# Optimization experiments

Measured on AMD Instinct MI355X. Metric: run time of the kernel, lower is better.

Reference implementation:

```python
import jax, jax.numpy as jnp
import numpy as np

BN_EPS = 1e-5

def _conv(x, w, bias=None):
    # x: [N,C,H,W], w: [O,I,3,3], SAME padding, stride 1
    y = jax.lax.conv_general_dilated(x, w, window_strides=(1, 1),
                                     padding=((1, 1), (1, 1)),
                                     dimension_numbers=('NCHW', 'OIHW', 'NCHW'))
    if bias is not None:
        y = y + bias[None, :, None, None]
    return y

def _cconv(xr, xi, wr, wi):
    # complex conv: (xr + i xi) * (wr + i wi), cross-term combination
    return _conv(xr, wr) - _conv(xi, wi), _conv(xr, wi) + _conv(xi, wr)

def _bn1(x, g, b):
    # per-channel batchnorm (training-style stats over N,H,W)
    mu = jnp.mean(x, axis=(0, 2, 3), keepdims=True)
    var = jnp.var(x, axis=(0, 2, 3), keepdims=True)
    xh = (x - mu) * jax.lax.rsqrt(var + BN_EPS)
    return xh * g[None, :, None, None] + b[None, :, None, None]

def _cbn(xr, xi, g, b):
    # naive complex BN: normalize real/imag parts separately, shared affine
    return _bn1(xr, g, b), _bn1(xi, g, b)

def _crelu(xr, xi):
    return jax.nn.relu(xr), jax.nn.relu(xi)

def setup_inputs() -> dict:
    key = jax.random.key(0)
    ks = jax.random.split(key, 16)
    def w(k, o, i, kh=3, kw=3, s=0.05):
        return jax.random.normal(k, (o, i, kh, kw), jnp.float32) * s
    d = {}
    d['x'] = jax.random.normal(ks[0], (4, 256, 128, 224), jnp.float32)
    d['w1r'] = w(ks[1], 144, 256); d['w1i'] = w(ks[2], 144, 256)
    d['g1'] = jnp.ones((144,), jnp.float32); d['b1'] = jnp.zeros((144,), jnp.float32)
    d['w2r'] = w(ks[3], 96, 144); d['w2i'] = w(ks[4], 96, 144)
    d['g2'] = jnp.ones((96,), jnp.float32); d['b2'] = jnp.zeros((96,), jnp.float32)
    d['w3r'] = w(ks[5], 96, 96); d['w3i'] = w(ks[6], 96, 96)
    d['g3'] = jnp.ones((96,), jnp.float32); d['b3'] = jnp.zeros((96,), jnp.float32)
    d['w4r'] = w(ks[7], 96, 96); d['w4i'] = w(ks[8], 96, 96)
    d['g4'] = jnp.ones((96,), jnp.float32); d['b4'] = jnp.zeros((96,), jnp.float32)
    d['wc'] = w(ks[9], 1, 96); d['bc'] = jnp.zeros((1,), jnp.float32)
    d['wg'] = w(ks[10], 2, 96); d['bg'] = jnp.zeros((2,), jnp.float32)
    return d

def reference(x, w1r, w1i, g1, b1, w2r, w2i, g2, b2,
              w3r, w3i, g3, b3, w4r, w4i, g4, b4, wc, bc, wg, bg):
    # real input promoted to complex with zero imag
    xr, xi = x, jnp.zeros_like(x)
    xr, xi = _cconv(xr, xi, w1r, w1i)
    xr, xi = _cbn(xr, xi, g1, b1)
    xr, xi = _crelu(xr, xi)
    xr, xi = _cconv(xr, xi, w2r, w2i)
    xr, xi = _cbn(xr, xi, g2, b2)
    xr, xi = _crelu(xr, xi)
    xr, xi = _cconv(xr, xi, w3r, w3i)
    xr, xi = _cbn(xr, xi, g3, b3)
    xr, xi = _crelu(xr, xi)
    xr, xi = _cconv(xr, xi, w4r, w4i)
    xr, xi = _cbn(xr, xi, g4, b4)
    xr, xi = _crelu(xr, xi)
    x_mag = jnp.sqrt(xr * xr + xi * xi)  # torch.abs on complex
    cls = jax.nn.sigmoid(_conv(x_mag, wc, bc))
    reg = _conv(x_mag, wg, bg)
    return jnp.concatenate([cls, reg], axis=1)  # [N, 1+reg_layer, H, W]
```

## Files before the change

### kernel.cpp

```cpp
#include <hip/hip_runtime.h>
#include <cstdint>
#include <cstddef>

#define P_TOT 114688
#define W_IMG 224
#define H_IMG 128
#define WP 228
#define HP 130

typedef _Float16 f16;
typedef __attribute__((ext_vector_type(8))) _Float16 f16x8;
typedef __attribute__((ext_vector_type(4))) _Float16 f16x4;
typedef __attribute__((ext_vector_type(4))) float f32x4;

#define WAITVM(N) asm volatile("s_waitcnt vmcnt(" #N ")" ::: "memory")

__device__ __forceinline__ void barrier_sync() {
  asm volatile("" ::: "memory");
  __builtin_amdgcn_s_barrier();
  asm volatile("" ::: "memory");
}

__device__ __forceinline__ void gload16(const void* g, void* l) {
  __builtin_amdgcn_global_load_lds((const __attribute__((address_space(1))) void*)g,
                                   (__attribute__((address_space(3))) void*)l, 16, 0, 0);
}

__device__ __forceinline__ size_t pad_px(int n, int h, int w) {
  return ((size_t)(n * HP + h + 1)) * WP + (w + 1);
}

__global__ void k_halo(f16* __restrict__ slab, int CS) {
  int c8n = CS >> 3;
  int tid = blockIdx.x * 256 + threadIdx.x;
  int c8 = tid % c8n;
  int rest = tid / c8n;
  if (rest >= 4 * 968) return;
  int n = rest / 968, i = rest % 968;
  int h, w;
  if (i < 456) { h = (i < 228) ? 0 : 129; w = i % 228; }
  else { int j = i - 456; h = 1 + (j >> 2); int k = j & 3; w = (k == 0) ? 0 : (224 + k); }
  size_t pp = ((size_t)(n * HP + h)) * WP + w;
  *(f16x8*)(slab + pp * CS + c8 * 8) = (f16x8){0, 0, 0, 0, 0, 0, 0, 0};
}

__global__ void k_pack_x(const float* __restrict__ x, f16* __restrict__ xb) {
  int tid = threadIdx.x;
  int pw  = tid & 15;
  int c8  = tid >> 4;
  int p   = blockIdx.x * 16 + pw;
  int w   = p % W_IMG;
  int h   = (p / W_IMG) % H_IMG;
  int n   = p / (H_IMG * W_IMG);
  const float* src = x + ((size_t)(n * 256 + c8 * 8) * H_IMG + h) * W_IMG + w;
  f16x8 v;
#pragma unroll
  for (int j = 0; j < 8; j++) v[j] = (f16)src[(size_t)j * (H_IMG * W_IMG)];
  int c8s = (c8 & ~3) | ((c8 ^ (w >> 1)) & 3);
  *(f16x8*)(xb + pad_px(n, h, w) * 256 + c8s * 8) = v;
}

__global__ void k_pack_w(const float* __restrict__ wa, const float* __restrict__ wb,
                         f16* __restrict__ dst, int mode, int OT, int CS,
                         int Coh, int Cih, int total) {
  int gid = blockIdx.x * 256 + threadIdx.x;
  if (gid >= total) return;
  int j  = gid & 31;
  int t1 = gid >> 5;
  int o  = t1 % OT;
  int t2 = t1 / OT;
  int CCc = CS >> 5;
  int cc = t2 % CCc;
  int kk = t2 / CCc;
  int chunkT = ((j >> 3) ^ (o >> 1)) & 3;
  int is = cc * 32 + chunkT * 8 + (j & 7);
  float val = 0.f;
  if (mode == 0) {
    val = (o < Coh) ? wa[((size_t)o * Cih + is) * 9 + kk]
                    : wb[((size_t)(o - Coh) * Cih + is) * 9 + kk];
  } else if (mode == 1) {
    if (o < Coh) {
      val = (is < Cih) ? wa[((size_t)o * Cih + is) * 9 + kk]
                       : -wb[((size_t)o * Cih + (is - Cih)) * 9 + kk];
    } else {
      int oo = o - Coh;
      val = (is < Cih) ? wb[((size_t)oo * Cih + is) * 9 + kk]
                       : wa[((size_t)oo * Cih + (is - Cih)) * 9 + kk];
    }
  } else {
    if (o == 0)      val = wa[(size_t)is * 9 + kk];
    else if (o == 1) val = wb[(size_t)is * 9 + kk];
    else if (o == 2) val = wb[(size_t)(96 + is) * 9 + kk];
  }
  dst[gid] = (f16)val;
}

template<int BM, int OT, int CS, int WM, int WN, bool HEAD>
__launch_bounds__(WM * WN * 64)
__global__ void k_gemm(const f16* __restrict__ xb, const f16* __restrict__ Apack,
                       f16* __restrict__ y, float* __restrict__ outh,
                       const float* __restrict__ bcp, const float* __restrict__ bgp,
                       float* __restrict__ sums, float* __restrict__ sumsq) {
  constexpr int NT = WM * WN * 64;
  constexpr int NWV = NT / 64;
  constexpr int CC = CS / 32;
  constexpr int MF = BM / (WM * 16);
  constexpr int NF = 224 / (WN * 16);
  constexpr int NCH = 9 * CC;
  constexpr int TILE1 = (BM + 224) * 32;
  constexpr int ACH = BM / 16;
  constexpr int TCH = ACH + 14;
  constexpr int NHALF = HEAD ? 1 : 2;
  static_assert(HEAD || (TCH % NWV == 0 && TCH / NWV == 5), "vmcnt math: 5 loads/thread/half");
  __shared__ f16 lds[2][NHALF * TILE1];

  constexpr int NOT = OT / BM;
  constexpr int nwg = NOT * 512;
  int bid = blockIdx.x;
  int swz = (bid & 7) * (nwg >> 3) + (bid >> 3);
  const int ot = swz % NOT;
  const int rq = swz / NOT;
  const int n = rq >> 7;
  const int h = rq & 127;
  const int tid  = threadIdx.x;
  const int lane = tid & 63;
  const int wv   = tid >> 6;
  const int wm   = wv % WM;
  const int wn   = wv / WM;
  const int obase  = wm * (MF * 16);
  const int wnbase = wn * (NF * 16);
  const int l15 = lane & 15;
  const int lhi = lane >> 4;
  const int aoff = l15 * 64 + (((lhi ^ (l15 >> 1)) & 3) << 4);

  f32x4 acc[MF][NF];
#pragma unroll
  for (int mi = 0; mi < MF; mi++)
#pragma unroll
    for (int ni = 0; ni < NF; ni++) acc[mi][ni] = (f32x4){0.f, 0.f, 0.f, 0.f};

  const char* abase = (const char*)Apack + (size_t)ot * BM * 64 + lane * 16;
  const char* bbase = (const char*)xb +
      (pad_px(n, h, 0) + (lane >> 2)) * (CS * 2) + (lane & 3) * 16;

  auto stage1 = [&](char* base, int q) {
    const int kk = q / CC, c = q % CC;
    const int dh = kk / 3 - 1;
    const int dw = kk % 3 - 1;
    const char* asrc = abase + (size_t)q * (OT * 64);
    const char* bsrc = bbase + (dh * WP + dw) * (int)(CS * 2) + c * 64;
#pragma unroll
    for (int ck = wv; ck < TCH; ck += NWV) {
      char* dst = base + ck * 1024;
      if (ck < ACH) gload16(asrc + ck * 1024, dst);
      else          gload16(bsrc + (size_t)(ck - ACH) * (16 * CS * 2), dst);
    }
  };

  auto compute_half = [&](const char* base, int kk) {
    const int dw = kk % 3 - 1;
    const char* Ab = base;
    const char* Bb = base + BM * 64;
    f16x8 af[MF], bfr[NF];
#pragma unroll
    for (int mi = 0; mi < MF; mi++)
      af[mi] = *(const f16x8*)(Ab + (obase + mi * 16) * 64 + aoff);
#pragma unroll
    for (int ni = 0; ni < NF; ni++) {
      int px = wnbase + ni * 16 + l15;
      int sw = ((lhi ^ ((px + dw) >> 1)) & 3) << 4;
      bfr[ni] = *(const f16x8*)(Bb + px * 64 + sw);
    }
    __builtin_amdgcn_s_setprio(1);
#pragma unroll
    for (int mi = 0; mi < MF; mi++)
#pragma unroll
      for (int ni = 0; ni < NF; ni++)
        acc[mi][ni] = __builtin_amdgcn_mfma_f32_16x16x32_f16(af[mi], bfr[ni], acc[mi][ni], 0, 0, 0);
    __builtin_amdgcn_s_setprio(0);
  };

  if constexpr (!HEAD) {
    constexpr int STEPS = (NCH + 1) / 2;
    auto stage_pair = [&](int buf, int q) {
      char* b = (char*)&lds[buf][0];
      int q1 = (q + 1 < NCH) ? (q + 1) : (NCH - 1);
      stage1(b, q);
      stage1(b + TILE1 * 2, q1);
    };
    stage_pair(0, 0);
    for (int s = 0; s < STEPS; ++s) {
      int qn = (s + 1) * 2;
      if (qn < NCH) { stage_pair((s + 1) & 1, qn); WAITVM(10); }
      else          { WAITVM(0); }
      barrier_sync();
      const char* b = (const char*)&lds[s & 1][0];
      int q = s * 2;
      compute_half(b, q / CC);
      if (q + 1 < NCH) compute_half(b + TILE1 * 2, (q + 1) / CC);
      barrier_sync();
    }
  } else {
    stage1((char*)&lds[0][0], 0);
    __syncthreads();
    int buf = 0;
    for (int t = 0; t < NCH; ++t) {
      int tn = t + 1;
      if (tn < NCH) stage1((char*)&lds[buf ^ 1][0], tn);
      compute_half((const char*)&lds[buf][0], t / CC);
      __syncthreads();
      buf ^= 1;
    }
  }

  if constexpr (!HEAD) {
    const size_t prow = pad_px(n, h, 0);
#pragma unroll
    for (int mi = 0; mi < MF; mi++) {
#pragma unroll
      for (int ni = 0; ni < NF; ni++) {
        int o = obase + mi * 16 + lhi * 4;
        int w = wnbase + ni * 16 + l15;
        f16x4 v4;
#pragma unroll
        for (int j = 0; j < 4; j++) v4[j] = (f16)acc[mi][ni][j];
        *(f16x4*)(y + (prow + w) * OT + ot * BM + o) = v4;
      }
    }
    float sv[MF][4], qv[MF][4];
#pragma unroll
    for (int mi = 0; mi < MF; mi++)
#pragma unroll
      for (int j = 0; j < 4; j++) {
        float s = 0.f, q = 0.f;
#pragma unroll
        for (int ni = 0; ni < NF; ni++) {
          float v = acc[mi][ni][j];
          s += v; q += v * v;
        }
        sv[mi][j] = s; qv[mi][j] = q;
      }
#pragma unroll
    for (int m = 1; m < 16; m <<= 1) {
#pragma unroll
      for (int mi = 0; mi < MF; mi++)
#pragma unroll
        for (int j = 0; j < 4; j++) {
          sv[mi][j] += __shfl_xor(sv[mi][j], m);
          qv[mi][j] += __shfl_xor(qv[mi][j], m);
        }
    }
    if (l15 == 0) {
#pragma unroll
      for (int mi = 0; mi < MF; mi++)
#pragma unroll
        for (int j = 0; j < 4; j++) {
          int ch = ot * BM + obase + mi * 16 + lhi * 4 + j;
          atomicAdd(&sums[ch], sv[mi][j]);
          atomicAdd(&sumsq[ch], qv[mi][j]);
        }
    }
  } else {
    if (lhi == 0) {
      float b0 = bcp[0], b1 = bgp[0], b2 = bgp[1];
#pragma unroll
      for (int ni = 0; ni < NF; ni++) {
        int w = wnbase + ni * 16 + l15;
        float c0 = acc[0][ni][0] + b0;
        c0 = 1.f / (1.f + expf(-c0));
        float c1 = acc[0][ni][1] + b1;
        float c2 = acc[0][ni][2] + b2;
        outh[((size_t)(n * 3 + 0) * H_IMG + h) * W_IMG + w] = c0;
        outh[((size_t)(n * 3 + 1) * H_IMG + h) * W_IMG + w] = c1;
        outh[((size_t)(n * 3 + 2) * H_IMG + h) * W_IMG + w] = c2;
      }
    }
  }
}

template<int O>
__device__ __forceinline__ void bn_coef(const float* __restrict__ sums,
                                        const float* __restrict__ sumsq,
                                        const float* __restrict__ g,
                                        const float* __restrict__ b,
                                        float* sc, float* sh, int tid, int nt) {
  const float inv = 1.0f / (float)P_TOT;
  for (int t = tid; t < O; t += nt) {
    float mean = sums[t] * inv;
    float var  = fmaxf(sumsq[t] * inv - mean * mean, 0.f);
    int gi = (t < O / 2) ? t : (t - O / 2);
    float s = g[gi] * rsqrtf(var + 1e-5f);
    sc[t] = s;
    sh[t] = b[gi] - mean * s;
  }
}

template<int O>
__global__ void k_packip(f16* __restrict__ y,
                         const float* __restrict__ sums, const float* __restrict__ sumsq,
                         const float* __restrict__ g, const float* __restrict__ b) {
  __shared__ float sc[O], sh[O];
  bn_coef<O>(sums, sumsq, g, b, sc, sh, threadIdx.x, 256);
  __syncthreads();
  constexpr int G32 = O / 32;
  int gid = blockIdx.x * 256 + threadIdx.x;
  if (gid >= P_TOT * G32) return;
  int gg = gid % G32;
  int p = gid / G32;
  int w = p % W_IMG;
  int hh = (p / W_IMG) % H_IMG;
  int nn = p / (W_IMG * H_IMG);
  f16* base = y + pad_px(nn, hh, w) * O + gg * 32;
  f16x8 in[4];
#pragma unroll
  for (int ch = 0; ch < 4; ch++) in[ch] = *(const f16x8*)(base + ch * 8);
  int sw = (w >> 1) & 3;
  f16x8 outv[4];
#pragma unroll
  for (int ch = 0; ch < 4; ch++) {
#pragma unroll
    for (int j = 0; j < 8; j++) {
      int cdx = gg * 32 + ch * 8 + j;
      float f = fmaxf(fmaf((float)in[ch][j], sc[cdx], sh[cdx]), 0.f);
      outv[ch][j] = (f16)f;
    }
  }
#pragma unroll
  for (int ch = 0; ch < 4; ch++) *(f16x8*)(base + ((ch ^ sw) & 3) * 8) = outv[ch];
}

__global__ void k_mag(const f16* __restrict__ y,
                      const float* __restrict__ sums, const float* __restrict__ sumsq,
                      const float* __restrict__ g, const float* __restrict__ b,
                      f16* __restrict__ mg) {
  __shared__ float sc[192], sh[192];
  bn_coef<192>(sums, sumsq, g, b, sc, sh, threadIdx.x, 256);
  __syncthreads();
  int gid = blockIdx.x * 256 + threadIdx.x;
  if (gid >= P_TOT * 12) return;
  int c8 = gid % 12;
  int p  = gid / 12;
  int w  = p % W_IMG;
  int hh = (p / W_IMG) % H_IMG;
  int nn = p / (W_IMG * H_IMG);
  size_t pp = pad_px(nn, hh, w);
  f16x8 r8 = *(const f16x8*)(y + pp * 192 + c8 * 8);
  f16x8 i8 = *(const f16x8*)(y + pp * 192 + 96 + c8 * 8);
  f16x8 outv;
#pragma unroll
  for (int j = 0; j < 8; j++) {
    int cdx = c8 * 8 + j;
    float rr = fmaxf(fmaf((float)r8[j], sc[cdx], sh[cdx]), 0.f);
    float ii = fmaxf(fmaf((float)i8[j], sc[96 + cdx], sh[96 + cdx]), 0.f);
    outv[j] = (f16)sqrtf(rr * rr + ii * ii);
  }
  int c8s = (c8 & ~3) | ((c8 ^ (w >> 1)) & 3);
  *(f16x8*)(mg + pp * 96 + c8s * 8) = outv;
}

extern "C" void kernel_launch(void* const* d_in, const int* in_sizes, int n_in,
                              void* d_out, int out_size, void* d_ws, size_t ws_size,
                              hipStream_t stream) {
  const float* x   = (const float*)d_in[0];
  const float* w1r = (const float*)d_in[1];
  const float* w1i = (const float*)d_in[2];
  const float* g1  = (const float*)d_in[3];
  const float* b1  = (const float*)d_in[4];
  const float* w2r = (const float*)d_in[5];
  const float* w2i = (const float*)d_in[6];
  const float* g2  = (const float*)d_in[7];
  const float* b2  = (const float*)d_in[8];
  const float* w3r = (const float*)d_in[9];
  const float* w3i = (const float*)d_in[10];
  const float* g3  = (const float*)d_in[11];
  const float* b3  = (const float*)d_in[12];
  const float* w4r = (const float*)d_in[13];
  const float* w4i = (const float*)d_in[14];
  const float* g4  = (const float*)d_in[15];
  const float* b4  = (const float*)d_in[16];
  const float* wc  = (const float*)d_in[17];
  const float* bcp = (const float*)d_in[18];
  const float* wg  = (const float*)d_in[19];
  const float* bgp = (const float*)d_in[20];
  float* out = (float*)d_out;

  char* ws = (char*)d_ws;
  if (ws_size < 137500000ULL) return;

  auto S  = [&](int L) { return (float*)(ws + 16384 + L * 4096); };
  auto Q  = [&](int L) { return (float*)(ws + 16384 + L * 4096) + 512; };
  f16* A1 = (f16*)(ws + 65536);
  f16* A2 = (f16*)(ws + 1392640);
  f16* A3 = (f16*)(ws + 2387968);
  f16* A4 = (f16*)(ws + 3051520);
  f16* AH = (f16*)(ws + 3715072);
  f16* SLA = (f16*)(ws + 4194304);
  f16* SLB = (f16*)(ws + 65011712);

  hipMemsetAsync(d_ws, 0, 49152, stream);

  auto halo_grid = [](int CS) { return (4 * 968 * (CS / 8) + 255) / 256; };

  k_halo<<<halo_grid(256), 256, 0, stream>>>(SLA, 256);
  k_pack_x<<<P_TOT / 16, 512, 0, stream>>>(x, SLA);
  k_pack_w<<<(663552 + 255) / 256, 256, 0, stream>>>(w1r, w1i, A1, 0, 288, 256, 144, 256, 663552);
  k_pack_w<<<(497664 + 255) / 256, 256, 0, stream>>>(w2r, w2i, A2, 1, 192, 288, 96, 144, 497664);
  k_pack_w<<<(331776 + 255) / 256, 256, 0, stream>>>(w3r, w3i, A3, 1, 192, 192, 96, 96, 331776);
  k_pack_w<<<(331776 + 255) / 256, 256, 0, stream>>>(w4r, w4i, A4, 1, 192, 192, 96, 96, 331776);
  k_pack_w<<<(13824 + 255) / 256, 256, 0, stream>>>(wc, wg, AH, 2, 16, 96, 0, 96, 13824);
  k_halo<<<halo_grid(288), 256, 0, stream>>>(SLB, 288);

  k_gemm<96, 288, 256, 2, 2, false><<<1536, 256, 0, stream>>>(SLA, A1, SLB, nullptr, nullptr, nullptr, S(0), Q(0));
  k_packip<288><<<P_TOT * 9 / 256, 256, 0, stream>>>(SLB, S(0), Q(0), g1, b1);
  k_halo<<<halo_grid(192), 256, 0, stream>>>(SLA, 192);

  k_gemm<96, 192, 288, 2, 2, false><<<1024, 256, 0, stream>>>(SLB, A2, SLA, nullptr, nullptr, nullptr, S(1), Q(1));
  k_packip<192><<<P_TOT * 6 / 256, 256, 0, stream>>>(SLA, S(1), Q(1), g2, b2);
  k_halo<<<halo_grid(192), 256, 0, stream>>>(SLB, 192);

  k_gemm<96, 192, 192, 2, 2, false><<<1024, 256, 0, stream>>>(SLA, A3, SLB, nullptr, nullptr, nullptr, S(2), Q(2));
  k_packip<192><<<P_TOT * 6 / 256, 256, 0, stream>>>(SLB, S(2), Q(2), g3, b3);

  k_gemm<96, 192, 192, 2, 2, false><<<1024, 256, 0, stream>>>(SLB, A4, SLA, nullptr, nullptr, nullptr, S(3), Q(3));
  k_halo<<<halo_grid(96), 256, 0, stream>>>(SLB, 96);

  k_mag<<<P_TOT * 12 / 256, 256, 0, stream>>>(SLA, S(3), Q(3), g4, b4, SLB);

  k_gemm<16, 16, 96, 1, 2, true><<<512, 128, 0, stream>>>(SLB, AH, nullptr, out, bcp, bgp, nullptr, nullptr);

  (void)in_sizes; (void)n_in; (void)out_size;
}
```

Baseline: 883.7 us.

## Replace paired double-buffer with 4-slot single-chunk pipeline in conv GEMM

The non-head conv GEMM loop moves from staging two K-chunks per step into a double buffer to a 4-slot ring of single chunks that prefetches three ahead. Each step reads its fragments from LDS before issuing the next global-to-LDS load, then waits on the counters and runs the MFMA cluster behind a sched_barrier. The aim is to hide global load latency and keep LDS reads off the critical path. The head kernel now stages only the single A chunk it needs, which shrinks its LDS footprint. The cost is an extra barrier per chunk, a larger LDS allocation that may lower occupancy, and hand-tuned vmcnt accounting that is fragile.

```diff
diff --git a/kernel.cpp b/kernel.cpp
--- a/kernel.cpp
+++ b/kernel.cpp
@@ -14,6 +14,7 @@
 typedef __attribute__((ext_vector_type(4))) float f32x4;
 
 #define WAITVM(N) asm volatile("s_waitcnt vmcnt(" #N ")" ::: "memory")
+#define WAITLGKM0() asm volatile("s_waitcnt lgkmcnt(0)" ::: "memory")
 
 __device__ __forceinline__ void barrier_sync() {
   asm volatile("" ::: "memory");
@@ -107,12 +108,12 @@
   constexpr int MF = BM / (WM * 16);
   constexpr int NF = 224 / (WN * 16);
   constexpr int NCH = 9 * CC;
-  constexpr int TILE1 = (BM + 224) * 32;
   constexpr int ACH = BM / 16;
   constexpr int TCH = ACH + 14;
-  constexpr int NHALF = HEAD ? 1 : 2;
-  static_assert(HEAD || (TCH % NWV == 0 && TCH / NWV == 5), "vmcnt math: 5 loads/thread/half");
-  __shared__ f16 lds[2][NHALF * TILE1];
+  constexpr int TILE1B = TCH * 1024;
+  constexpr int LDS_BYTES = HEAD ? (2 * 15 * 1024) : (4 * TILE1B);
+  static_assert(HEAD || (TCH % NWV == 0 && TCH / NWV == 5), "vmcnt math: 5 loads/thread/chunk");
+  __shared__ __align__(16) char lds[LDS_BYTES];
 
   constexpr int NOT = OT / BM;
   constexpr int nwg = NOT * 512;
@@ -141,14 +142,13 @@
 
   const char* abase = (const char*)Apack + (size_t)ot * BM * 64 + lane * 16;
   const char* bbase = (const char*)xb +
-      (pad_px(n, h, 0) + (lane >> 2)) * (CS * 2) + (lane & 3) * 16;
+      (pad_px(n, h, 0) + (lane >> 2)) * (size_t)(CS * 2) + (lane & 3) * 16;
 
   auto stage1 = [&](char* base, int q) {
     const int kk = q / CC, c = q % CC;
-    const int dh = kk / 3 - 1;
-    const int dw = kk % 3 - 1;
+    const int doff = (kk / 3 - 1) * WP + (kk % 3 - 1);
     const char* asrc = abase + (size_t)q * (OT * 64);
-    const char* bsrc = bbase + (dh * WP + dw) * (int)(CS * 2) + c * 64;
+    const char* bsrc = bbase + (ptrdiff_t)doff * (CS * 2) + c * 64;
 #pragma unroll
     for (int ck = wv; ck < TCH; ck += NWV) {
       char* dst = base + ck * 1024;
@@ -157,11 +157,10 @@
     }
   };
 
-  auto compute_half = [&](const char* base, int kk) {
-    const int dw = kk % 3 - 1;
+  auto read_frags = [&](const char* base, int q, f16x8* af, f16x8* bfr) {
+    const int dw = (q / CC) % 3 - 1;
     const char* Ab = base;
-    const char* Bb = base + BM * 64;
-    f16x8 af[MF], bfr[NF];
+    const char* Bb = base + ACH * 1024;
 #pragma unroll
     for (int mi = 0; mi < MF; mi++)
       af[mi] = *(const f16x8*)(Ab + (obase + mi * 16) * 64 + aoff);
@@ -171,6 +170,9 @@
       int sw = ((lhi ^ ((px + dw) >> 1)) & 3) << 4;
       bfr[ni] = *(const f16x8*)(Bb + px * 64 + sw);
     }
+  };
+
+  auto mfma_cluster = [&](const f16x8* af, const f16x8* bfr) {
     __builtin_amdgcn_s_setprio(1);
 #pragma unroll
     for (int mi = 0; mi < MF; mi++)
@@ -181,40 +183,51 @@
   };
 
   if constexpr (!HEAD) {
-    constexpr int STEPS = (NCH + 1) / 2;
-    auto stage_pair = [&](int buf, int q) {
-      char* b = (char*)&lds[buf][0];
-      int q1 = (q + 1 < NCH) ? (q + 1) : (NCH - 1);
-      stage1(b, q);
-      stage1(b + TILE1 * 2, q1);
+    f16x8 af[MF], bfr[NF];
+    stage1(lds + 0 * TILE1B, 0);
+    stage1(lds + 1 * TILE1B, 1);
+    stage1(lds + 2 * TILE1B, 2);
+    WAITVM(10);
+    barrier_sync();
+    for (int t = 0; t < NCH; ++t) {
+      read_frags(lds + (t & 3) * TILE1B, t, af, bfr);
+      if (t + 3 < NCH) { stage1(lds + ((t + 3) & 3) * TILE1B, t + 3); WAITVM(10); }
+      else if (t + 3 == NCH) { WAITVM(5); }
+      else if (t + 2 == NCH) { WAITVM(0); }
+      barrier_sync();
+      WAITLGKM0();
+      __builtin_amdgcn_sched_barrier(0);
+      mfma_cluster(af, bfr);
+      barrier_sync();
+    }
+  } else {
+    constexpr int HTCH = 1 + 14;
+    auto stage_blk = [&](char* base, int q) {
+      const int kk = q / CC, c = q % CC;
+      const int doff = (kk / 3 - 1) * WP + (kk % 3 - 1);
+      const char* asrc = abase + (size_t)q * (OT * 64);
+      const char* bsrc = bbase + (ptrdiff_t)doff * (CS * 2) + c * 64;
+      for (int ck = wv; ck < HTCH; ck += NWV) {
+        char* dst = base + ck * 1024;
+        if (ck < 1) gload16(asrc, dst);
+        else        gload16(bsrc + (size_t)(ck - 1) * (16 * CS * 2), dst);
+      }
     };
-    stage_pair(0, 0);
-    for (int s = 0; s < STEPS; ++s) {
-      int qn = (s + 1) * 2;
-      if (qn < NCH) { stage_pair((s + 1) & 1, qn); WAITVM(10); }
-      else          { WAITVM(0); }
-      barrier_sync();
-      const char* b = (const char*)&lds[s & 1][0];
-      int q = s * 2;
-      compute_half(b, q / CC);
-      if (q + 1 < NCH) compute_half(b + TILE1 * 2, (q + 1) / CC);
-      barrier_sync();
-    }
-  } else {
-    stage1((char*)&lds[0][0], 0);
+    f16x8 af[MF], bfr[NF];
+    stage_blk(lds, 0);
     __syncthreads();
     int buf = 0;
     for (int t = 0; t < NCH; ++t) {
-      int tn = t + 1;
-      if (tn < NCH) stage1((char*)&lds[buf ^ 1][0], tn);
-      compute_half((const char*)&lds[buf][0], t / CC);
+      if (t + 1 < NCH) stage_blk(lds + (buf ^ 1) * 15360, t + 1);
+      read_frags(lds + buf * 15360, t, af, bfr);
+      mfma_cluster(af, bfr);
       __syncthreads();
       buf ^= 1;
     }
   }
 
+  const size_t prow = pad_px(n, h, 0);
   if constexpr (!HEAD) {
-    const size_t prow = pad_px(n, h, 0);
 #pragma unroll
     for (int mi = 0; mi < MF; mi++) {
 #pragma unroll
```

New measurement: 941.3 us. +6.5%, slower.
